# Optimization experiments

Measured on AMD Instinct MI355X. Metric: run time of the kernel, lower is better.

## Reference

```python
import jax, jax.numpy as jnp
import numpy as np

B = 8192
D_IN = 10
H = 1900


def _l2norm_cols(w):
    # tf.nn.l2_normalize(w, dim=0): normalize each column, eps 1e-12
    sq = jnp.sum(w * w, axis=0, keepdims=True)
    return w * jax.lax.rsqrt(jnp.maximum(sq, 1e-12))


def setup_inputs() -> dict:
    key = jax.random.key(0)
    ks = jax.random.split(key, 12)
    return {
        "inputs": jax.random.normal(ks[0], (B, D_IN), jnp.float32),
        "c_prev": jax.random.normal(ks[1], (B, H), jnp.float32),
        "h_prev": jax.random.normal(ks[2], (B, H), jnp.float32),
        "wx": jax.random.normal(ks[3], (D_IN, 4 * H), jnp.float32) * 0.1,
        "wh": jax.random.normal(ks[4], (H, 4 * H), jnp.float32) * 0.1,
        "wmx": jax.random.normal(ks[5], (D_IN, H), jnp.float32) * 0.1,
        "wmh": jax.random.normal(ks[6], (H, H), jnp.float32) * 0.1,
        "b": jax.random.normal(ks[7], (4 * H,), jnp.float32) * 0.1,
        "gx": jax.random.uniform(ks[8], (4 * H,), jnp.float32, 0.5, 1.5),
        "gh": jax.random.uniform(ks[9], (4 * H,), jnp.float32, 0.5, 1.5),
        "gmx": jax.random.uniform(ks[10], (H,), jnp.float32, 0.5, 1.5),
        "gmh": jax.random.uniform(ks[11], (H,), jnp.float32, 0.5, 1.5),
    }


def reference(inputs, c_prev, h_prev, wx, wh, wmx, wmh, b, gx, gh, gmx, gmh):
    # weight-normalized weights (per-column l2 norm * gain)
    wx_n = _l2norm_cols(wx) * gx
    wh_n = _l2norm_cols(wh) * gh
    wmx_n = _l2norm_cols(wmx) * gmx
    wmh_n = _l2norm_cols(wmh) * gmh
    # multiplicative state m: [B, H]
    m = (inputs @ wmx_n) * (h_prev @ wmh_n)
    # gate pre-activations z: [B, 4H]
    z = inputs @ wx_n + m @ wh_n + b
    i, f, o, u = jnp.split(z, 4, axis=1)
    i = jax.nn.sigmoid(i)
    f = jax.nn.sigmoid(f)
    o = jax.nn.sigmoid(o)
    u = jnp.tanh(u)
    c = f * c_prev + i * u
    h = o * jnp.tanh(c)
    return (h, c)
```

## Files before the change

kernel.cpp:

```cpp
#include <hip/hip_runtime.h>

typedef unsigned short ushort_t;
typedef short bf16x8 __attribute__((ext_vector_type(8)));
typedef float f32x4 __attribute__((ext_vector_type(4)));

#define H 1900
#define FH 7600
#define BATCH 8192
#define KP 1952
#define NP_A 1920
#define NB 7680
#define BK 32
#define KITERS (KP / BK)

#define NKT 30
#define KT_U 16384
#define TAIL_U 491520
#define PANEL_U 499712

static const size_t OFF_SWX  = 0;
static const size_t OFF_SWH  = 32768;
static const size_t OFF_SWMX = 65536;
static const size_t OFF_SWMH = 73728;
static const size_t OFF_WMXN = 81920;
static const size_t OFF_PART = 163840;
static const size_t OFF_HBF  = 786432;
static const size_t OFF_MEXT = OFF_HBF + 31981568;
static const size_t OFF_WMHT = OFF_MEXT + 31981568;
static const size_t OFF_WHXT = OFF_WMHT + 7495680;

#define PW_X  0
#define PW_H  60800
#define PW_MX 121600
#define PW_MH 136800

#define BAR() __builtin_amdgcn_s_barrier()
#define PRIO1 __builtin_amdgcn_s_setprio(1)
#define PRIO0 __builtin_amdgcn_s_setprio(0)
#define WAIT_LGKM0 asm volatile("s_waitcnt lgkmcnt(0)" ::: "memory")
#define WAIT_VM(N) asm volatile("s_waitcnt vmcnt(" #N ")" ::: "memory")

__device__ __forceinline__ ushort_t f2bf(float x) {
  unsigned u = __float_as_uint(x);
  return (ushort_t)((u + 0x7fffu + ((u >> 16) & 1u)) >> 16);
}

__device__ __forceinline__ void gl_lds16(const ushort_t* g, ushort_t* lds) {
  __builtin_amdgcn_global_load_lds(
      (const __attribute__((address_space(1))) unsigned int*)(g),
      (__attribute__((address_space(3))) unsigned int*)(lds), 16, 0, 0);
}

__device__ __forceinline__ size_t tiled_addr(int row, int col) {
  return (size_t)(row >> 8) * PANEL_U + (size_t)(col >> 6) * KT_U +
         (size_t)(row & 255) * 64 + (col & 63);
}
__device__ __forceinline__ size_t tiled_addr_tail(int row, int ctail) {
  return (size_t)(row >> 8) * PANEL_U + TAIL_U + (size_t)(row & 255) * 32 + ctail;
}

__global__ void colsum_partial_kernel(const float* __restrict__ wx, const float* __restrict__ wh,
                                      const float* __restrict__ wmx, const float* __restrict__ wmh,
                                      float* __restrict__ parts) {
  int c = blockIdx.x * 256 + threadIdx.x;
  int y = blockIdx.y, p = blockIdx.z;
  const float* W; int K, N; float* out;
  if (y == 0)      { W = wx;  K = 10;   N = FH; out = parts + PW_X  + (size_t)p * FH; }
  else if (y == 1) { W = wh;  K = 1900; N = FH; out = parts + PW_H  + (size_t)p * FH; }
  else if (y == 2) { W = wmx; K = 10;   N = H;  out = parts + PW_MX + (size_t)p * H;  }
  else             { W = wmh; K = 1900; N = H;  out = parts + PW_MH + (size_t)p * H;  }
  if (c >= N) return;
  int rp = (K + 7) / 8;
  int r0 = p * rp, r1 = r0 + rp; if (r1 > K) r1 = K;
  float s = 0.f;
  for (int r = r0; r < r1; ++r) { float v = W[(size_t)r * N + c]; s += v * v; }
  out[c] = s;
}

__global__ void scales_final_kernel(const float* __restrict__ parts,
                                    const float* __restrict__ gx, const float* __restrict__ gh,
                                    const float* __restrict__ gmx, const float* __restrict__ gmh,
                                    float* __restrict__ s_wx, float* __restrict__ s_wh,
                                    float* __restrict__ s_wmx, float* __restrict__ s_wmh) {
  int c = blockIdx.x * 256 + threadIdx.x;
  int y = blockIdx.y;
  const float* pp; int N; const float* g; float* out;
  if (y == 0)      { pp = parts + PW_X;  N = FH; g = gx;  out = s_wx;  }
  else if (y == 1) { pp = parts + PW_H;  N = FH; g = gh;  out = s_wh;  }
  else if (y == 2) { pp = parts + PW_MX; N = H;  g = gmx; out = s_wmx; }
  else             { pp = parts + PW_MH; N = H;  g = gmh; out = s_wmh; }
  if (c >= N) return;
  float s = 0.f;
  for (int p = 0; p < 8; ++p) s += pp[(size_t)p * N + c];
  out[c] = g[c] * rsqrtf(fmaxf(s, 1e-12f));
}

__global__ void cvt_h_kernel(const float* __restrict__ h_prev, ushort_t* __restrict__ hbf) {
  size_t idx = (size_t)blockIdx.x * 256 + threadIdx.x;
  int row = (int)(idx / KP), col = (int)(idx % KP);
  float v = (col < H) ? h_prev[(size_t)row * H + col] : 0.f;
  hbf[idx] = f2bf(v);
}

__global__ void wmxn_kernel(const float* __restrict__ wmx, const float* __restrict__ s_wmx,
                            float* __restrict__ wmxn) {
  int idx = blockIdx.x * 256 + threadIdx.x;
  int i = idx / NP_A, j = idx - i * NP_A;
  wmxn[idx] = (j < H) ? wmx[i * H + j] * s_wmx[j] : 0.f;
}

__global__ void wmhT_kernel(const float* __restrict__ wmh, const float* __restrict__ s_wmh,
                            ushort_t* __restrict__ wmhT) {
  __shared__ float tile[32][33];
  int n0 = blockIdx.x * 32, k0 = blockIdx.y * 32;
  int tx = threadIdx.x & 31, ty = threadIdx.x >> 5;
#pragma unroll
  for (int it = 0; it < 4; ++it) {
    int k = k0 + ty + it * 8, n = n0 + tx;
    float v = (k < H && n < H) ? wmh[(size_t)k * H + n] : 0.f;
    tile[ty + it * 8][tx] = v;
  }
  __syncthreads();
#pragma unroll
  for (int it = 0; it < 4; ++it) {
    int n = n0 + ty + it * 8, k = k0 + tx;
    float v = tile[tx][ty + it * 8];
    float s = (n < H) ? s_wmh[n] : 0.f;
    wmhT[(size_t)n * KP + k] = f2bf(v * s);
  }
}

__global__ void whxT_kernel(const float* __restrict__ wh, const float* __restrict__ wx,
                            const float* __restrict__ s_wh, const float* __restrict__ s_wx,
                            ushort_t* __restrict__ whxT) {
  __shared__ float tile[32][33];
  int c0 = blockIdx.x * 32, k0 = blockIdx.y * 32;
  int tx = threadIdx.x & 31, ty = threadIdx.x >> 5;
#pragma unroll
  for (int it = 0; it < 4; ++it) {
    int k = k0 + ty + it * 8, c = c0 + tx;
    float v = 0.f;
    if (c < FH) {
      if (k < H) v = wh[(size_t)k * FH + c] * s_wh[c];
      else if (k >= NP_A && k < NP_A + 10) v = wx[(size_t)(k - NP_A) * FH + c] * s_wx[c];
    }
    tile[ty + it * 8][tx] = v;
  }
  __syncthreads();
#pragma unroll
  for (int it = 0; it < 4; ++it) {
    int c = c0 + ty + it * 8, k = k0 + tx;
    if (c < FH) {
      int g = c / H; int j = c - g * H; int n = 4 * j + g;
      size_t a = (k < NP_A) ? tiled_addr(n, k) : tiled_addr_tail(n, k - NP_A);
      whxT[a] = f2bf(tile[tx][ty + it * 8]);
    }
  }
}

__global__ void mext_tail_kernel(const float* __restrict__ inputs, ushort_t* __restrict__ m_ext) {
  int idx = blockIdx.x * 256 + threadIdx.x;
  int row = idx >> 5, c = idx & 31;
  float v = (c < 10) ? inputs[(size_t)row * 10 + c] : 0.f;
  m_ext[tiled_addr_tail(row, c)] = f2bf(v);
}

__global__ void whxT_tail_kernel(ushort_t* __restrict__ whxT) {
  int idx = blockIdx.x * 256 + threadIdx.x;
  int n = 7600 + idx / 1952, k = idx % 1952;
  size_t a = (k < NP_A) ? tiled_addr(n, k) : tiled_addr_tail(n, k - NP_A);
  whxT[a] = 0;
}

__device__ __forceinline__ void gemm_tile128(const ushort_t* __restrict__ Ag,
                                             const ushort_t* __restrict__ Bg,
                                             int m0, int n0,
                                             ushort_t* As, ushort_t* Bs,
                                             f32x4 acc[4][4]) {
  const int tid = threadIdx.x;
  const int lane = tid & 63;
  const int quad = lane >> 4;
  const int lo = lane & 15;
  const int wave = tid >> 6;
  const int wm = (wave & 1) << 6;
  const int wn = (wave >> 1) << 6;
  const int sw = (lo >> 1) & 3;

  const int cr = lane >> 2;
  const int hg = (lane & 3) ^ ((lane >> 3) & 3);
  const int r0 = wave * 16 + cr;
  const int r1 = 64 + wave * 16 + cr;
  const ushort_t* gA0 = Ag + (size_t)(m0 + r0) * KP + hg * 8;
  const ushort_t* gA1 = Ag + (size_t)(m0 + r1) * KP + hg * 8;
  const ushort_t* gB0 = Bg + (size_t)(n0 + r0) * KP + hg * 8;
  const ushort_t* gB1 = Bg + (size_t)(n0 + r1) * KP + hg * 8;
  ushort_t* lA0 = As + (wave * 16) * BK;
  ushort_t* lA1 = As + (64 + wave * 16) * BK;
  ushort_t* lB0 = Bs + (wave * 16) * BK;
  ushort_t* lB1 = Bs + (64 + wave * 16) * BK;

  for (int kt = 0; kt < KITERS; ++kt) {
    __syncthreads();
    gl_lds16(gA0, lA0);
    gl_lds16(gA1, lA1);
    gl_lds16(gB0, lB0);
    gl_lds16(gB1, lB1);
    __syncthreads();
    bf16x8 af[4], bfv[4];
#pragma unroll
    for (int mf = 0; mf < 4; ++mf)
      af[mf] = *(const bf16x8*)(As + (wm + mf * 16 + lo) * BK + ((quad ^ sw) << 3));
#pragma unroll
    for (int nf = 0; nf < 4; ++nf)
      bfv[nf] = *(const bf16x8*)(Bs + (wn + nf * 16 + lo) * BK + ((quad ^ sw) << 3));
#pragma unroll
    for (int mf = 0; mf < 4; ++mf)
#pragma unroll
      for (int nf = 0; nf < 4; ++nf)
        acc[mf][nf] = __builtin_amdgcn_mfma_f32_16x16x32_bf16(af[mf], bfv[nf], acc[mf][nf], 0, 0, 0);
    gA0 += BK; gA1 += BK; gB0 += BK; gB1 += BK;
  }
}

__global__ void __launch_bounds__(256) gemmA_kernel(const ushort_t* __restrict__ hbf,
                                                    const ushort_t* __restrict__ wmhT,
                                                    const float* __restrict__ inputs,
                                                    const float* __restrict__ wmxn,
                                                    ushort_t* __restrict__ m_ext) {
  __shared__ __align__(16) char smem[16384];
  ushort_t* As = (ushort_t*)smem;
  ushort_t* Bs = (ushort_t*)(smem + 8192);
  f32x4 acc[4][4];
  f32x4 zv = {0.f, 0.f, 0.f, 0.f};
#pragma unroll
  for (int a = 0; a < 4; ++a)
#pragma unroll
    for (int bq = 0; bq < 4; ++bq) acc[a][bq] = zv;
  int m0 = blockIdx.x * 128, n0 = blockIdx.y * 128;
  gemm_tile128(hbf, wmhT, m0, n0, As, Bs, acc);
  __syncthreads();
  float* inL  = (float*)smem;
  float* wmxL = (float*)(smem + 5120);
  for (int t = threadIdx.x; t < 1280; t += 256) {
    int r = t / 10, i = t - r * 10;
    inL[t] = inputs[(size_t)(m0 + r) * 10 + i];
  }
  for (int t = threadIdx.x; t < 1280; t += 256) {
    int i = t >> 7, c = t & 127;
    wmxL[t] = wmxn[i * NP_A + n0 + c];
  }
  __syncthreads();
  const int lane = threadIdx.x & 63, quad = lane >> 4, lo = lane & 15;
  const int wave = threadIdx.x >> 6, wm = (wave & 1) << 6, wn = (wave >> 1) << 6;
#pragma unroll
  for (int mf = 0; mf < 4; ++mf)
#pragma unroll
    for (int r = 0; r < 4; ++r) {
      int rl = wm + mf * 16 + quad * 4 + r;
      float inrow[10];
#pragma unroll
      for (int i = 0; i < 10; ++i) inrow[i] = inL[rl * 10 + i];
#pragma unroll
      for (int nf = 0; nf < 4; ++nf) {
        int cl = wn + nf * 16 + lo;
        float mx = 0.f;
#pragma unroll
        for (int i = 0; i < 10; ++i) mx += inrow[i] * wmxL[i * 128 + cl];
        float mv = acc[mf][nf][r] * mx;
        m_ext[tiled_addr(m0 + rl, n0 + cl)] = f2bf(mv);
      }
    }
}


__device__ __forceinline__ void stage_half(const ushort_t* __restrict__ Gp, int rbase, int kt,
                                           ushort_t* L, int tid) {
  const int wave = tid >> 6;
#pragma unroll
  for (int q = 0; q < 2; ++q) {
    const int idx = q * 512 + tid;
    const int r = idx >> 3, s = idx & 7;
    const int gs = s ^ (r & 7);
    gl_lds16(Gp + (size_t)kt * KT_U + (size_t)(rbase + r) * 64 + gs * 8,
             L + (size_t)(q * 512 + wave * 64) * 8);
  }
}

__device__ __forceinline__ void read_Ahalf(const ushort_t* A, int wmL, int lo, int mh,
                                           int sw0, int sw1, bf16x8 af[8]) {
#pragma unroll
  for (int mf = 0; mf < 4; ++mf) {
    const ushort_t* p = A + ((wmL + mh * 64 + mf * 16 + lo) << 6);
    af[mf * 2 + 0] = *(const bf16x8*)(p + sw0);
    af[mf * 2 + 1] = *(const bf16x8*)(p + sw1);
  }
}

__device__ __forceinline__ void read_Bhalf(const ushort_t* B, int wnL, int lo, int nh,
                                           int sw0, int sw1, bf16x8 bf[4]) {
#pragma unroll
  for (int nf = 0; nf < 2; ++nf) {
    const ushort_t* p = B + ((wnL + nh * 32 + nf * 16 + lo) << 6);
    bf[nf * 2 + 0] = *(const bf16x8*)(p + sw0);
    bf[nf * 2 + 1] = *(const bf16x8*)(p + sw1);
  }
}

__device__ __forceinline__ void mfma_quad(const bf16x8 af[8], const bf16x8 bf[4],
                                          f32x4 acc[8][4], int mh, int nh) {
#pragma unroll
  for (int mf = 0; mf < 4; ++mf)
#pragma unroll
    for (int nf = 0; nf < 2; ++nf) {
      f32x4 c = acc[mh * 4 + mf][nh * 2 + nf];
      c = __builtin_amdgcn_mfma_f32_16x16x32_bf16(af[mf * 2 + 0], bf[nf * 2 + 0], c, 0, 0, 0);
      c = __builtin_amdgcn_mfma_f32_16x16x32_bf16(af[mf * 2 + 1], bf[nf * 2 + 1], c, 0, 0, 0);
      acc[mh * 4 + mf][nh * 2 + nf] = c;
    }
}

template <int MODE>
__device__ __forceinline__ void b8_iter(const ushort_t* __restrict__ Ap,
                                        const ushort_t* __restrict__ Bp,
                                        int T,
                                        ushort_t* Acur, ushort_t* Bcur,
                                        ushort_t* Anxt, ushort_t* Bnxt,
                                        int tid, int lo, int wmL, int wnL,
                                        int sw0, int sw1, f32x4 acc[8][4]) {
  bf16x8 af[8], b0f[4], b1f[4];
  read_Ahalf(Acur, wmL, lo, 0, sw0, sw1, af);
  read_Bhalf(Bcur, wnL, lo, 0, sw0, sw1, b0f);
  if (MODE <= 1) stage_half(Ap, 128, T + 1, Anxt + 8192, tid);
  BAR(); WAIT_LGKM0;
  PRIO1; mfma_quad(af, b0f, acc, 0, 0); PRIO0;
  BAR();
  read_Bhalf(Bcur, wnL, lo, 1, sw0, sw1, b1f);
  BAR(); WAIT_LGKM0;
  PRIO1; mfma_quad(af, b1f, acc, 0, 1); PRIO0;
  BAR();
  read_Ahalf(Acur, wmL, lo, 1, sw0, sw1, af);
  if (MODE == 0) stage_half(Bp, 0, T + 2, Bcur, tid);
  BAR(); WAIT_LGKM0;
  PRIO1; mfma_quad(af, b1f, acc, 1, 1); PRIO0;
  BAR();
  if (MODE == 0) {
    stage_half(Ap, 0, T + 2, Acur, tid);
    stage_half(Bp, 128, T + 2, Bcur + 8192, tid);
    WAIT_VM(6);
  } else if (MODE == 1) {
    WAIT_VM(0);
  }
  BAR();
  PRIO1; mfma_quad(af, b0f, acc, 1, 0); PRIO0;
  BAR();
}

__global__ void __launch_bounds__(512, 2)
gemmB8_kernel(const ushort_t* __restrict__ mext, const ushort_t* __restrict__ whxT,
              const float* __restrict__ bvec, const float* __restrict__ c_prev,
              float* __restrict__ hout, float* __restrict__ cout) {
  extern __shared__ __align__(16) char smem[];
  ushort_t* As0 = (ushort_t*)smem;
  ushort_t* Bs0 = (ushort_t*)(smem + 32768);
  ushort_t* As1 = (ushort_t*)(smem + 65536);
  ushort_t* Bs1 = (ushort_t*)(smem + 98304);

  const int tid = threadIdx.x;
  const int lane = tid & 63;
  const int lo = lane & 15, quad = lane >> 4;
  const int wave = tid >> 6;
  const int wmL = (wave & 1) << 7;
  const int wnL = (wave >> 1) << 6;
  const int sw0 = ((quad ^ (lo & 7)) << 3);
  const int sw1 = (((4 | quad) ^ (lo & 7)) << 3);

  int bid = blockIdx.x;
  int xcd = bid & 7, j = bid >> 3;
  int mt = ((xcd & 3) << 3) | (j & 7);
  int nt = (xcd >> 2) * 15 + (j >> 3);
  int m0 = mt << 8, n0 = nt << 8;

  f32x4 acc[8][4];
  f32x4 zv = {0.f, 0.f, 0.f, 0.f};
#pragma unroll
  for (int a = 0; a < 8; ++a)
#pragma unroll
    for (int bq = 0; bq < 4; ++bq) acc[a][bq] = zv;

  const ushort_t* Ap = mext + (size_t)mt * PANEL_U;
  const ushort_t* Bp = whxT + (size_t)nt * PANEL_U;

  stage_half(Ap, 0,   0, As0,        tid);
  stage_half(Bp, 0,   0, Bs0,        tid);
  stage_half(Ap, 128, 0, As0 + 8192, tid);
  stage_half(Bp, 128, 0, Bs0 + 8192, tid);
  stage_half(Bp, 0,   1, Bs1,        tid);
  stage_half(Ap, 0,   1, As1,        tid);
  stage_half(Bp, 128, 1, Bs1 + 8192, tid);
  WAIT_VM(6);
  BAR();

  for (int T = 0; T < NKT - 2; T += 2) {
    b8_iter<0>(Ap, Bp, T,     As0, Bs0, As1, Bs1, tid, lo, wmL, wnL, sw0, sw1, acc);
    b8_iter<0>(Ap, Bp, T + 1, As1, Bs1, As0, Bs0, tid, lo, wmL, wnL, sw0, sw1, acc);
  }
  b8_iter<1>(Ap, Bp, NKT - 2, As0, Bs0, As1, Bs1, tid, lo, wmL, wnL, sw0, sw1, acc);
  b8_iter<2>(Ap, Bp, NKT - 1, As1, Bs1, As0, Bs0, tid, lo, wmL, wnL, sw0, sw1, acc);

  {
    const int wavei = tid >> 6;
#pragma unroll
    for (int q = 0; q < 2; ++q) {
      const int idx = q * 512 + tid;
      const int r = idx >> 2, s = idx & 3;
      const int gs = s ^ (r & 3);
      gl_lds16(Ap + TAIL_U + (size_t)r * 32 + gs * 8,
               As0 + (size_t)(q * 512 + wavei * 64) * 8);
    }
#pragma unroll
    for (int q = 0; q < 2; ++q) {
      const int idx = q * 512 + tid;
      const int r = idx >> 2, s = idx & 3;
      const int gs = s ^ (r & 3);
      gl_lds16(Bp + TAIL_U + (size_t)r * 32 + gs * 8,
               Bs0 + (size_t)(q * 512 + wavei * 64) * 8);
    }
    WAIT_VM(0);
    BAR();
    const int swt = ((quad ^ (lo & 3)) << 3);
    bf16x8 a2[8], b2[4];
#pragma unroll
    for (int mf = 0; mf < 8; ++mf)
      a2[mf] = *(const bf16x8*)(As0 + ((wmL + mf * 16 + lo) << 5) + swt);
#pragma unroll
    for (int nf = 0; nf < 4; ++nf)
      b2[nf] = *(const bf16x8*)(Bs0 + ((wnL + nf * 16 + lo) << 5) + swt);
#pragma unroll
    for (int mf = 0; mf < 8; ++mf)
#pragma unroll
      for (int nf = 0; nf < 4; ++nf)
        acc[mf][nf] = __builtin_amdgcn_mfma_f32_16x16x32_bf16(a2[mf], b2[nf], acc[mf][nf], 0, 0, 0);
  }

#pragma unroll
  for (int nf = 0; nf < 4; ++nf) {
    int gn = n0 + wnL + nf * 16 + lo;
    int j2 = gn >> 2, g = gn & 3;
    float bias = (j2 < H) ? bvec[g * H + j2] : 0.f;
#pragma unroll
    for (int mf = 0; mf < 8; ++mf)
#pragma unroll
      for (int r = 0; r < 4; ++r) {
        float zs = acc[mf][nf][r] + bias;
        float v1 = __shfl_xor(zs, 1);
        float v2 = __shfl_xor(zs, 2);
        float v3 = __shfl_xor(v1, 2);
        if (g == r && j2 < H) {
          float zi, zf, zo, zu;
          { int t = 0 ^ g; zi = t == 0 ? zs : t == 1 ? v1 : t == 2 ? v2 : v3; }
          { int t = 1 ^ g; zf = t == 0 ? zs : t == 1 ? v1 : t == 2 ? v2 : v3; }
          { int t = 2 ^ g; zo = t == 0 ? zs : t == 1 ? v1 : t == 2 ? v2 : v3; }
          { int t = 3 ^ g; zu = t == 0 ? zs : t == 1 ? v1 : t == 2 ? v2 : v3; }
          float iv = 1.f / (1.f + __expf(-zi));
          float fv = 1.f / (1.f + __expf(-zf));
          float ov = 1.f / (1.f + __expf(-zo));
          float uv = tanhf(zu);
          int row = m0 + wmL + mf * 16 + quad * 4 + r;
          size_t oidx = (size_t)row * H + j2;
          float cp = c_prev[oidx];
          float cv = fv * cp + iv * uv;
          hout[oidx] = ov * tanhf(cv);
          cout[oidx] = cv;
        }
      }
  }
}

extern "C" void kernel_launch(void* const* d_in, const int* in_sizes, int n_in,
                              void* d_out, int out_size, void* d_ws, size_t ws_size,
                              hipStream_t stream) {
  const float* inputs = (const float*)d_in[0];
  const float* c_prev = (const float*)d_in[1];
  const float* h_prev = (const float*)d_in[2];
  const float* wx  = (const float*)d_in[3];
  const float* wh  = (const float*)d_in[4];
  const float* wmx = (const float*)d_in[5];
  const float* wmh = (const float*)d_in[6];
  const float* bv  = (const float*)d_in[7];
  const float* gx  = (const float*)d_in[8];
  const float* gh  = (const float*)d_in[9];
  const float* gmx = (const float*)d_in[10];
  const float* gmh = (const float*)d_in[11];

  char* ws = (char*)d_ws;
  float* s_wx  = (float*)(ws + OFF_SWX);
  float* s_wh  = (float*)(ws + OFF_SWH);
  float* s_wmx = (float*)(ws + OFF_SWMX);
  float* s_wmh = (float*)(ws + OFF_SWMH);
  float* wmxn  = (float*)(ws + OFF_WMXN);
  float* parts = (float*)(ws + OFF_PART);
  ushort_t* hbf   = (ushort_t*)(ws + OFF_HBF);
  ushort_t* m_ext = (ushort_t*)(ws + OFF_MEXT);
  ushort_t* wmhT  = (ushort_t*)(ws + OFF_WMHT);
  ushort_t* whxT  = (ushort_t*)(ws + OFF_WHXT);

  float* hout = (float*)d_out;
  float* cout = hout + (size_t)BATCH * H;

  static bool attr_set = false;
  if (!attr_set) {
    hipFuncSetAttribute(reinterpret_cast<const void*>(&gemmB8_kernel),
                        hipFuncAttributeMaxDynamicSharedMemorySize, 131072);
    attr_set = true;
  }

  colsum_partial_kernel<<<dim3(30, 4, 8), 256, 0, stream>>>(wx, wh, wmx, wmh, parts);
  scales_final_kernel<<<dim3(30, 4), 256, 0, stream>>>(parts, gx, gh, gmx, gmh,
                                                       s_wx, s_wh, s_wmx, s_wmh);
  cvt_h_kernel<<<62464, 256, 0, stream>>>(h_prev, hbf);
  wmxn_kernel<<<75, 256, 0, stream>>>(wmx, s_wmx, wmxn);
  wmhT_kernel<<<dim3(60, 61), 256, 0, stream>>>(wmh, s_wmh, wmhT);
  whxT_kernel<<<dim3(238, 61), 256, 0, stream>>>(wh, wx, s_wh, s_wx, whxT);
  mext_tail_kernel<<<1024, 256, 0, stream>>>(inputs, m_ext);
  whxT_tail_kernel<<<610, 256, 0, stream>>>(whxT);
  gemmA_kernel<<<dim3(64, 15), 256, 0, stream>>>(hbf, wmhT, inputs, wmxn, m_ext);
  gemmB8_kernel<<<dim3(960), 512, 131072, stream>>>(m_ext, whxT, bv, c_prev, hout, cout);
}
```

Measured before the change: 1.052 ms.

## Restructure GEMM main loop into two barrier phases with early LDS reads

Reworks the per-k-tile schedule of the big GEMM. All A and B fragments are read from LDS up front, and the MFMA work is split into two larger groups separated by only two barriers instead of four. Refills of B and A for tile T+2 go directly into the current buffers after their reads complete, and the tail-K loads are issued inside the last iteration so they overlap compute. This cuts barrier and waitcnt overhead but holds more fragment registers live (a0 and a1 together), which may add register pressure at 2 blocks per CU.

```diff
diff --git a/kernel.cpp b/kernel.cpp
--- a/kernel.cpp
+++ b/kernel.cpp
@@ -37,7 +37,8 @@
 #define BAR() __builtin_amdgcn_s_barrier()
 #define PRIO1 __builtin_amdgcn_s_setprio(1)
 #define PRIO0 __builtin_amdgcn_s_setprio(0)
-#define WAIT_LGKM0 asm volatile("s_waitcnt lgkmcnt(0)" ::: "memory")
+#define SB0() __builtin_amdgcn_sched_barrier(0)
+#define WAIT_LGKM(N) asm volatile("s_waitcnt lgkmcnt(" #N ")" ::: "memory")
 #define WAIT_VM(N) asm volatile("s_waitcnt vmcnt(" #N ")" ::: "memory")
 
 __device__ __forceinline__ ushort_t f2bf(float x) {
@@ -286,6 +287,18 @@
   }
 }
 
+__device__ __forceinline__ void stage_tail(const ushort_t* __restrict__ Gp, ushort_t* L, int tid) {
+  const int wave = tid >> 6;
+#pragma unroll
+  for (int q = 0; q < 2; ++q) {
+    const int idx = q * 512 + tid;
+    const int r = idx >> 2, s = idx & 3;
+    const int gs = s ^ (r & 3);
+    gl_lds16(Gp + TAIL_U + (size_t)r * 32 + gs * 8,
+             L + (size_t)(q * 512 + wave * 64) * 8);
+  }
+}
+
 __device__ __forceinline__ void read_Ahalf(const ushort_t* A, int wmL, int lo, int mh,
                                            int sw0, int sw1, bf16x8 af[8]) {
 #pragma unroll
@@ -320,38 +333,50 @@
 }
 
 template <int MODE>
-__device__ __forceinline__ void b8_iter(const ushort_t* __restrict__ Ap,
+__device__ __forceinline__ void b8_tile(const ushort_t* __restrict__ Ap,
                                         const ushort_t* __restrict__ Bp,
                                         int T,
                                         ushort_t* Acur, ushort_t* Bcur,
-                                        ushort_t* Anxt, ushort_t* Bnxt,
+                                        ushort_t* tailA, ushort_t* tailB,
                                         int tid, int lo, int wmL, int wnL,
                                         int sw0, int sw1, f32x4 acc[8][4]) {
-  bf16x8 af[8], b0f[4], b1f[4];
-  read_Ahalf(Acur, wmL, lo, 0, sw0, sw1, af);
+  bf16x8 a0[8], a1[8], b0f[4], b1f[4];
+  read_Ahalf(Acur, wmL, lo, 0, sw0, sw1, a0);
   read_Bhalf(Bcur, wnL, lo, 0, sw0, sw1, b0f);
-  if (MODE <= 1) stage_half(Ap, 128, T + 1, Anxt + 8192, tid);
-  BAR(); WAIT_LGKM0;
-  PRIO1; mfma_quad(af, b0f, acc, 0, 0); PRIO0;
-  BAR();
   read_Bhalf(Bcur, wnL, lo, 1, sw0, sw1, b1f);
-  BAR(); WAIT_LGKM0;
-  PRIO1; mfma_quad(af, b1f, acc, 0, 1); PRIO0;
-  BAR();
-  read_Ahalf(Acur, wmL, lo, 1, sw0, sw1, af);
-  if (MODE == 0) stage_half(Bp, 0, T + 2, Bcur, tid);
-  BAR(); WAIT_LGKM0;
-  PRIO1; mfma_quad(af, b1f, acc, 1, 1); PRIO0;
+  SB0();
+  read_Ahalf(Acur, wmL, lo, 1, sw0, sw1, a1);
+  SB0();
+  WAIT_LGKM(8);
+  SB0();
+  PRIO1;
+  mfma_quad(a0, b0f, acc, 0, 0);
+  mfma_quad(a0, b1f, acc, 0, 1);
+  PRIO0;
   BAR();
   if (MODE == 0) {
-    stage_half(Ap, 0, T + 2, Acur, tid);
+    stage_half(Bp, 0,   T + 2, Bcur, tid);
     stage_half(Bp, 128, T + 2, Bcur + 8192, tid);
-    WAIT_VM(6);
+  } else if (MODE == 2) {
+    stage_tail(Ap, tailA, tid);
+  }
+  WAIT_LGKM(0);
+  SB0();
+  PRIO1;
+  mfma_quad(a1, b1f, acc, 1, 1);
+  mfma_quad(a1, b0f, acc, 1, 0);
+  PRIO0;
+  BAR();
+  if (MODE == 0) {
+    stage_half(Ap, 0,   T + 2, Acur, tid);
+    stage_half(Ap, 128, T + 2, Acur + 8192, tid);
+    WAIT_VM(8);
   } else if (MODE == 1) {
     WAIT_VM(0);
-  }
-  BAR();
-  PRIO1; mfma_quad(af, b0f, acc, 1, 0); PRIO0;
+  } else {
+    stage_tail(Bp, tailB, tid);
+    WAIT_VM(0);
+  }
   BAR();
 }
 
@@ -375,9 +400,9 @@
   const int sw1 = (((4 | quad) ^ (lo & 7)) << 3);
 
   int bid = blockIdx.x;
-  int xcd = bid & 7, j = bid >> 3;
-  int mt = ((xcd & 3) << 3) | (j & 7);
-  int nt = (xcd >> 2) * 15 + (j >> 3);
+  int xcd = bid & 7, jj = bid >> 3;
+  int mt = ((xcd & 3) << 3) | (jj & 7);
+  int nt = (xcd >> 2) * 15 + (jj >> 3);
   int m0 = mt << 8, n0 = nt << 8;
 
   f32x4 acc[8][4];
@@ -391,42 +416,24 @@
   const ushort_t* Bp = whxT + (size_t)nt * PANEL_U;
 
   stage_half(Ap, 0,   0, As0,        tid);
+  stage_half(Ap, 128, 0, As0 + 8192, tid);
   stage_half(Bp, 0,   0, Bs0,        tid);
-  stage_half(Ap, 128, 0, As0 + 8192, tid);
   stage_half(Bp, 128, 0, Bs0 + 8192, tid);
+  stage_half(Ap, 0,   1, As1,        tid);
+  stage_half(Ap, 128, 1, As1 + 8192, tid);
   stage_half(Bp, 0,   1, Bs1,        tid);
-  stage_half(Ap, 0,   1, As1,        tid);
   stage_half(Bp, 128, 1, Bs1 + 8192, tid);
-  WAIT_VM(6);
+  WAIT_VM(8);
   BAR();
 
   for (int T = 0; T < NKT - 2; T += 2) {
-    b8_iter<0>(Ap, Bp, T,     As0, Bs0, As1, Bs1, tid, lo, wmL, wnL, sw0, sw1, acc);
-    b8_iter<0>(Ap, Bp, T + 1, As1, Bs1, As0, Bs0, tid, lo, wmL, wnL, sw0, sw1, acc);
-  }
-  b8_iter<1>(Ap, Bp, NKT - 2, As0, Bs0, As1, Bs1, tid, lo, wmL, wnL, sw0, sw1, acc);
-  b8_iter<2>(Ap, Bp, NKT - 1, As1, Bs1, As0, Bs0, tid, lo, wmL, wnL, sw0, sw1, acc);
+    b8_tile<0>(Ap, Bp, T,     As0, Bs0, As0, Bs0, tid, lo, wmL, wnL, sw0, sw1, acc);
+    b8_tile<0>(Ap, Bp, T + 1, As1, Bs1, As0, Bs0, tid, lo, wmL, wnL, sw0, sw1, acc);
+  }
+  b8_tile<1>(Ap, Bp, NKT - 2, As0, Bs0, As0, Bs0, tid, lo, wmL, wnL, sw0, sw1, acc);
+  b8_tile<2>(Ap, Bp, NKT - 1, As1, Bs1, As0, Bs0, tid, lo, wmL, wnL, sw0, sw1, acc);
 
   {
-    const int wavei = tid >> 6;
-#pragma unroll
-    for (int q = 0; q < 2; ++q) {
-      const int idx = q * 512 + tid;
-      const int r = idx >> 2, s = idx & 3;
-      const int gs = s ^ (r & 3);
-      gl_lds16(Ap + TAIL_U + (size_t)r * 32 + gs * 8,
-               As0 + (size_t)(q * 512 + wavei * 64) * 8);
-    }
-#pragma unroll
-    for (int q = 0; q < 2; ++q) {
-      const int idx = q * 512 + tid;
-      const int r = idx >> 2, s = idx & 3;
-      const int gs = s ^ (r & 3);
-      gl_lds16(Bp + TAIL_U + (size_t)r * 32 + gs * 8,
-               Bs0 + (size_t)(q * 512 + wavei * 64) * 8);
-    }
-    WAIT_VM(0);
-    BAR();
     const int swt = ((quad ^ (lo & 3)) << 3);
     bf16x8 a2[8], b2[4];
 #pragma unroll
```

After: 1.609 ms. 52.9% more time.
